# Performance work log

Measured on AMD Instinct MI355X. Metric: run time of the kernel, lower is better.

The kernel has to match this reference:

```python
import jax, jax.numpy as jnp
import numpy as np

N = 100000   # nodes
E = 1600000  # edges
B = 128      # graphs
VOCAB, EMB, HID = 10000, 128, 128


def gcn_conv(x, src, dst, ew, W, b, n_nodes):
    # PyG GCNConv: x' = D^{-1/2}(A_w + I) D^{-1/2} (x W) + b, self-loop weight 1
    x = x @ W  # [N, H]
    loop = jnp.arange(n_nodes)
    src2 = jnp.concatenate([src, loop])
    dst2 = jnp.concatenate([dst, loop])
    ew2 = jnp.concatenate([ew, jnp.ones((n_nodes,), x.dtype)])
    deg = jax.ops.segment_sum(ew2, dst2, num_segments=n_nodes)
    dinv = jnp.where(deg > 0, deg ** -0.5, 0.0)
    norm = dinv[src2] * ew2 * dinv[dst2]                      # [E+N]
    msg = x[src2] * norm[:, None]                             # gather-scale
    out = jax.ops.segment_sum(msg, dst2, num_segments=n_nodes)  # scatter-add
    return out + b


def setup_inputs() -> dict:
    key = jax.random.key(0)
    ks = jax.random.split(key, 12)
    x_idx = jax.random.randint(ks[0], (N,), 0, VOCAB)
    edge_index = jax.random.randint(ks[1], (2, E), 0, N)
    edge_weight = jax.random.uniform(ks[2], (E,), jnp.float32)
    batch = jnp.sort(jax.random.randint(ks[3], (N,), 0, B))
    emb_table = jax.random.normal(ks[4], (VOCAB, EMB), jnp.float32)
    emb_table = emb_table.at[0].set(0.0)  # padding_idx=0
    s = 1.0 / np.sqrt(EMB)
    W1 = jax.random.uniform(ks[5], (EMB, HID), jnp.float32, -s, s)
    b1 = jnp.zeros((HID,), jnp.float32)
    W2 = jax.random.uniform(ks[6], (HID, HID), jnp.float32, -s, s)
    b2 = jnp.zeros((HID,), jnp.float32)
    mlp_W1 = jax.random.uniform(ks[7], (HID, HID // 2), jnp.float32, -s, s)
    mlp_b1 = jax.random.uniform(ks[8], (HID // 2,), jnp.float32, -s, s)
    s2 = 1.0 / np.sqrt(HID // 2)
    mlp_W2 = jax.random.uniform(ks[9], (HID // 2, 2), jnp.float32, -s2, s2)
    mlp_b2 = jax.random.uniform(ks[10], (2,), jnp.float32, -s2, s2)
    return dict(x_idx=x_idx, edge_index=edge_index, edge_weight=edge_weight,
                batch=batch, emb_table=emb_table, W1=W1, b1=b1, W2=W2, b2=b2,
                mlp_W1=mlp_W1, mlp_b1=mlp_b1, mlp_W2=mlp_W2, mlp_b2=mlp_b2)


def reference(x_idx, edge_index, edge_weight, batch, emb_table, W1, b1, W2, b2,
              mlp_W1, mlp_b1, mlp_W2, mlp_b2):
    src, dst = edge_index[0], edge_index[1]
    x = emb_table[x_idx]                                  # embedding lookup
    x = jax.nn.relu(gcn_conv(x, src, dst, edge_weight, W1, b1, N))
    # dropout is inference no-op
    x = jax.nn.relu(gcn_conv(x, src, dst, edge_weight, W2, b2, N))
    # global mean pool over graphs
    sums = jax.ops.segment_sum(x, batch, num_segments=B)
    cnts = jax.ops.segment_sum(jnp.ones((N,), x.dtype), batch, num_segments=B)
    g = sums / jnp.maximum(cnts, 1.0)[:, None]            # [B, HID]
    h = jax.nn.relu(g @ mlp_W1 + mlp_b1)
    out = h @ mlp_W2 + mlp_b2
    return jax.nn.softmax(out, axis=1)
```

## Files before the change

kernel.cpp:

```cpp
#include <hip/hip_runtime.h>
#include <hip/hip_bf16.h>

#define NN 100000
#define NE 1600000
#define NB 128
#define NV 10000
#define HD 128

#define NBUCK 391
#define EBLK 256
#define EPB (NE / EBLK)

using bf16x8 = __attribute__((ext_vector_type(8))) short;
using f32x4  = __attribute__((ext_vector_type(4))) float;
typedef __attribute__((ext_vector_type(8))) unsigned short ushortv8;
typedef __attribute__((ext_vector_type(8))) unsigned char ucharv8;
typedef float f32x2 __attribute__((ext_vector_type(2)));

__device__ __forceinline__ float bf2f(unsigned short b) {
  return __uint_as_float((unsigned)b << 16);
}
__device__ __forceinline__ unsigned short f2bf(float f) {
  __hip_bfloat16 h = __float2bfloat16(f);
  return *reinterpret_cast<unsigned short*>(&h);
}
__device__ __forceinline__ unsigned char f2fp8(float f) {
  return (unsigned char)(__builtin_amdgcn_cvt_pk_fp8_f32(f, 0.f, 0, false) & 0xff);
}
__device__ __forceinline__ void acc16(float* acc, uint4 u, float c) {
  f32x2 v;
  v = __builtin_amdgcn_cvt_pk_f32_fp8((int)u.x, false); acc[0] += c*v[0]; acc[1] += c*v[1];
  v = __builtin_amdgcn_cvt_pk_f32_fp8((int)u.x, true);  acc[2] += c*v[0]; acc[3] += c*v[1];
  v = __builtin_amdgcn_cvt_pk_f32_fp8((int)u.y, false); acc[4] += c*v[0]; acc[5] += c*v[1];
  v = __builtin_amdgcn_cvt_pk_f32_fp8((int)u.y, true);  acc[6] += c*v[0]; acc[7] += c*v[1];
  v = __builtin_amdgcn_cvt_pk_f32_fp8((int)u.z, false); acc[8] += c*v[0]; acc[9] += c*v[1];
  v = __builtin_amdgcn_cvt_pk_f32_fp8((int)u.z, true);  acc[10]+= c*v[0]; acc[11]+= c*v[1];
  v = __builtin_amdgcn_cvt_pk_f32_fp8((int)u.w, false); acc[12]+= c*v[0]; acc[13]+= c*v[1];
  v = __builtin_amdgcn_cvt_pk_f32_fp8((int)u.w, true);  acc[14]+= c*v[0]; acc[15]+= c*v[1];
}


__global__ __launch_bounds__(256) void k_bcount(const int* __restrict__ dst,
                                                int* __restrict__ cntmat) {
  __shared__ int h[NBUCK];
  int t = threadIdx.x, blk = blockIdx.x;
  for (int i = t; i < NBUCK; i += 256) h[i] = 0;
  __syncthreads();
  int base = blk * EPB;
  for (int i = t; i < EPB; i += 256) atomicAdd(&h[dst[base + i] >> 8], 1);
  __syncthreads();
  for (int i = t; i < NBUCK; i += 256) cntmat[blk * NBUCK + i] = h[i];
}

__global__ __launch_bounds__(256) void k_cscan(int* __restrict__ cntmat,
                                               int* __restrict__ totals) {
  __shared__ int sh[256];
  int bu = blockIdx.x, t = threadIdx.x;
  int v = cntmat[t * NBUCK + bu];
  sh[t] = v;
  __syncthreads();
  #pragma unroll
  for (int off = 1; off < 256; off <<= 1) {
    int u = (t >= off) ? sh[t - off] : 0;
    __syncthreads();
    sh[t] += u;
    __syncthreads();
  }
  cntmat[t * NBUCK + bu] = sh[t] - v;
  if (t == 255) totals[bu] = sh[255];
}

__global__ __launch_bounds__(512) void k_tscan(const int* __restrict__ totals,
                                               int* __restrict__ bucketBase) {
  __shared__ int sh[512];
  int t = threadIdx.x;
  int v = (t < NBUCK) ? totals[t] : 0;
  sh[t] = v;
  __syncthreads();
  #pragma unroll
  for (int off = 1; off < 512; off <<= 1) {
    int u = (t >= off) ? sh[t - off] : 0;
    __syncthreads();
    sh[t] += u;
    __syncthreads();
  }
  if (t < NBUCK) bucketBase[t] = sh[t] - v;
  if (t == NBUCK - 1) bucketBase[NBUCK] = sh[t];
}

__global__ __launch_bounds__(256) void k_bscatter(const int* __restrict__ src,
                                                  const int* __restrict__ dst,
                                                  const float* __restrict__ ew,
                                                  const int* __restrict__ cntmat,
                                                  const int* __restrict__ bucketBase,
                                                  unsigned char* __restrict__ dloc,
                                                  uint2* __restrict__ spair) {
  __shared__ int off[NBUCK];
  int t = threadIdx.x, blk = blockIdx.x;
  for (int i = t; i < NBUCK; i += 256)
    off[i] = bucketBase[i] + cntmat[blk * NBUCK + i];
  __syncthreads();
  int base = blk * EPB;
  for (int i = t; i < EPB; i += 256) {
    int e = base + i;
    int d = dst[e];
    int pos = atomicAdd(&off[d >> 8], 1);
    dloc[pos] = (unsigned char)(d & 255);
    spair[pos] = make_uint2((unsigned)src[e], __float_as_uint(ew[e]));
  }
}

__global__ __launch_bounds__(256) void k_bdeg(const unsigned char* __restrict__ dloc,
                                              const uint2* __restrict__ spair,
                                              const int* __restrict__ bucketBase,
                                              int* __restrict__ rowptr,
                                              float* __restrict__ dinv) {
  __shared__ int cnt[256];
  __shared__ float ws[256];
  __shared__ int sh[256];
  int bu = blockIdx.x, t = threadIdx.x;
  cnt[t] = 0; ws[t] = 0.f;
  __syncthreads();
  int ebeg = bucketBase[bu], eend = bucketBase[bu + 1];
  for (int e = ebeg + t; e < eend; e += 256) {
    int dl = dloc[e];
    atomicAdd(&cnt[dl], 1);
    atomicAdd(&ws[dl], __uint_as_float(spair[e].y));
  }
  __syncthreads();
  int v = cnt[t];
  sh[t] = v;
  __syncthreads();
  #pragma unroll
  for (int off = 1; off < 256; off <<= 1) {
    int u = (t >= off) ? sh[t - off] : 0;
    __syncthreads();
    sh[t] += u;
    __syncthreads();
  }
  int gid = bu * 256 + t;
  if (gid < NN) {
    rowptr[gid] = ebeg + sh[t] - v;
    dinv[gid] = rsqrtf(1.0f + ws[t]);
  }
  if (gid == NN) rowptr[NN] = NE;
}

__global__ __launch_bounds__(256) void k_bfill(const unsigned char* __restrict__ dloc,
                                               const uint2* __restrict__ spair,
                                               const int* __restrict__ bucketBase,
                                               const int* __restrict__ rowptr,
                                               const float* __restrict__ dinv,
                                               uint2* __restrict__ csr) {
  __shared__ int cnt[256];
  __shared__ float sdv[256];
  __shared__ int srp[256];
  int bu = blockIdx.x, t = threadIdx.x;
  cnt[t] = 0;
  int gid = (bu << 8) + t;
  if (gid < NN) { sdv[t] = dinv[gid]; srp[t] = rowptr[gid]; }
  __syncthreads();
  int ebeg = bucketBase[bu], eend = bucketBase[bu + 1];
  for (int e = ebeg + t; e < eend; e += 256) {
    int dl = dloc[e];
    uint2 p = spair[e];
    int r = atomicAdd(&cnt[dl], 1);
    float nrm = dinv[(int)p.x] * __uint_as_float(p.y) * sdv[dl];
    csr[srp[dl] + r] = make_uint2(p.x, __float_as_uint(nrm));
  }
}

__global__ void k_wprep2(const float* __restrict__ W1, const float* __restrict__ W2,
                         unsigned short* __restrict__ Wt1, unsigned short* __restrict__ Wt2) {
  int t = blockIdx.x * blockDim.x + threadIdx.x;
  const float* W = (t < 16384) ? W1 : W2;
  unsigned short* Wt = (t < 16384) ? Wt1 : Wt2;
  int i = t & 16383;
  int k = i >> 7, n = i & 127;
  Wt[n * 128 + k] = f2bf(W[k * 128 + n]);
}

template <bool AF32>
__global__ __launch_bounds__(256) void k_gemm_mfma(const void* __restrict__ Av,
                                                   const unsigned short* __restrict__ Wt,
                                                   unsigned char* __restrict__ C, int M) {
  __shared__ unsigned char Cs[128][132];
  const int t = threadIdx.x;
  const int wave = t >> 6, lane = t & 63;
  const int lrow = lane & 15, lk = lane >> 4;
  const int row0 = blockIdx.x * 128;
  const int wrow = row0 + wave * 32;

  f32x4 acc[2][8];
  #pragma unroll
  for (int i = 0; i < 2; ++i)
    #pragma unroll
    for (int j = 0; j < 8; ++j) acc[i][j] = (f32x4){0.f, 0.f, 0.f, 0.f};

  #pragma unroll
  for (int kt = 0; kt < 4; ++kt) {
    bf16x8 a[2];
    #pragma unroll
    for (int rt = 0; rt < 2; ++rt) {
      int r = wrow + rt * 16 + lrow;
      bf16x8 av = (bf16x8){0, 0, 0, 0, 0, 0, 0, 0};
      if (r < M) {
        if (AF32) {
          const float* ap = (const float*)Av + (size_t)r * HD + kt * 32 + lk * 8;
          #pragma unroll
          for (int j = 0; j < 8; ++j) av[j] = (short)f2bf(ap[j]);
        } else {
          av = *(const bf16x8*)((const unsigned short*)Av + (size_t)r * HD + kt * 32 + lk * 8);
        }
      }
      a[rt] = av;
    }
    #pragma unroll
    for (int ct = 0; ct < 8; ++ct) {
      bf16x8 b = *(const bf16x8*)(Wt + (size_t)(ct * 16 + lrow) * HD + kt * 32 + lk * 8);
      acc[0][ct] = __builtin_amdgcn_mfma_f32_16x16x32_bf16(a[0], b, acc[0][ct], 0, 0, 0);
      acc[1][ct] = __builtin_amdgcn_mfma_f32_16x16x32_bf16(a[1], b, acc[1][ct], 0, 0, 0);
    }
  }

  #pragma unroll
  for (int rt = 0; rt < 2; ++rt)
    #pragma unroll
    for (int ct = 0; ct < 8; ++ct)
      #pragma unroll
      for (int reg = 0; reg < 4; ++reg) {
        int lr = wave * 32 + rt * 16 + lk * 4 + reg;
        Cs[lr][ct * 16 + lrow] = f2fp8(acc[rt][ct][reg]);
      }
  __syncthreads();

  #pragma unroll
  for (int i = 0; i < 8; ++i) {
    int idx = t + i * 256;
    int r = idx >> 4;
    int c = (idx & 15) * 8;
    int gr = row0 + r;
    if (gr < M)
      *(ucharv8*)(C + (size_t)gr * HD + c) = *(const ucharv8*)&Cs[r][c];
  }
}

template <bool IND, bool POOL>
__global__ __launch_bounds__(256) void k_agg8(const unsigned char* __restrict__ xw,
                                              const int* __restrict__ xidx,
                                              const int* __restrict__ rowptr,
                                              const uint2* __restrict__ csr,
                                              const float* __restrict__ dinv,
                                              const float* __restrict__ bias,
                                              unsigned short* __restrict__ outp,
                                              const int* __restrict__ batch,
                                              float* __restrict__ sums) {
  int t = threadIdx.x;
  int n = blockIdx.x * 32 + (t >> 3);
  int lane = t & 7;
  int beg = rowptr[n], end = rowptr[n + 1];

  int sn = IND ? xidx[n] : n;
  uint4 uself = *(const uint4*)(xw + (size_t)sn * HD + lane * 16);

  float acc[16];
  #pragma unroll
  for (int j = 0; j < 16; ++j) acc[j] = 0.f;

  int e = beg;
  for (; e + 3 < end; e += 4) {
    uint2 p0 = csr[e],     p1 = csr[e + 1];
    uint2 p2 = csr[e + 2], p3 = csr[e + 3];
    int s0 = (int)p0.x, s1 = (int)p1.x, s2 = (int)p2.x, s3 = (int)p3.x;
    if (IND) { s0 = xidx[s0]; s1 = xidx[s1]; s2 = xidx[s2]; s3 = xidx[s3]; }
    float c0 = __uint_as_float(p0.y), c1 = __uint_as_float(p1.y);
    float c2 = __uint_as_float(p2.y), c3 = __uint_as_float(p3.y);
    uint4 u0 = *(const uint4*)(xw + (size_t)s0 * HD + lane * 16);
    uint4 u1 = *(const uint4*)(xw + (size_t)s1 * HD + lane * 16);
    uint4 u2 = *(const uint4*)(xw + (size_t)s2 * HD + lane * 16);
    uint4 u3 = *(const uint4*)(xw + (size_t)s3 * HD + lane * 16);
    acc16(acc, u0, c0); acc16(acc, u1, c1);
    acc16(acc, u2, c2); acc16(acc, u3, c3);
  }
  for (; e < end; ++e) {
    uint2 p0 = csr[e];
    int s0 = (int)p0.x;
    float c0 = __uint_as_float(p0.y);
    if (IND) s0 = xidx[s0];
    uint4 u0 = *(const uint4*)(xw + (size_t)s0 * HD + lane * 16);
    acc16(acc, u0, c0);
  }

  float d = dinv[n];
  acc16(acc, uself, d * d);

  const float4* bp = reinterpret_cast<const float4*>(bias + lane * 16);
  float4 b0 = bp[0], b1 = bp[1], b2 = bp[2], b3 = bp[3];
  float o[16];
  o[0]  = fmaxf(acc[0]  + b0.x, 0.f); o[1]  = fmaxf(acc[1]  + b0.y, 0.f);
  o[2]  = fmaxf(acc[2]  + b0.z, 0.f); o[3]  = fmaxf(acc[3]  + b0.w, 0.f);
  o[4]  = fmaxf(acc[4]  + b1.x, 0.f); o[5]  = fmaxf(acc[5]  + b1.y, 0.f);
  o[6]  = fmaxf(acc[6]  + b1.z, 0.f); o[7]  = fmaxf(acc[7]  + b1.w, 0.f);
  o[8]  = fmaxf(acc[8]  + b2.x, 0.f); o[9]  = fmaxf(acc[9]  + b2.y, 0.f);
  o[10] = fmaxf(acc[10] + b2.z, 0.f); o[11] = fmaxf(acc[11] + b2.w, 0.f);
  o[12] = fmaxf(acc[12] + b3.x, 0.f); o[13] = fmaxf(acc[13] + b3.y, 0.f);
  o[14] = fmaxf(acc[14] + b3.z, 0.f); o[15] = fmaxf(acc[15] + b3.w, 0.f);

  if constexpr (!POOL) {
    ushortv8 r0, r1;
    #pragma unroll
    for (int j = 0; j < 8; ++j) { r0[j] = f2bf(o[j]); r1[j] = f2bf(o[8 + j]); }
    *(ushortv8*)(outp + (size_t)n * HD + lane * 16) = r0;
    *(ushortv8*)(outp + (size_t)n * HD + lane * 16 + 8) = r1;
  } else {
    __shared__ float pool[32][129];
    __shared__ int ib[32];
    int nl = t >> 3;
    #pragma unroll
    for (int j = 0; j < 16; ++j) pool[nl][lane * 16 + j] = o[j];
    if (t < 32) ib[t] = batch[blockIdx.x * 32 + t];
    __syncthreads();
    if (t < 128) {
      float a = 0.f;
      int c = t;
      #pragma unroll 4
      for (int i = 0; i < 32; ++i) {
        a += pool[i][c];
        if (i == 31 || ib[i + 1] != ib[i]) {
          atomicAdd(&sums[(size_t)ib[i] * HD + c], a);
          a = 0.f;
        }
      }
    }
  }
}

__global__ __launch_bounds__(256) void k_zero_counts(float* __restrict__ sums,
                                                     const int* __restrict__ batch,
                                                     float* __restrict__ cnt) {
  int i = blockIdx.x * blockDim.x + threadIdx.x;
  if (i < NB * HD) sums[i] = 0.f;
  if (blockIdx.x == 0 && threadIdx.x < NB) {
    int b = threadIdx.x;
    auto lb = [&](int v) {
      int lo = 0, hi = NN;
      while (lo < hi) { int m = (lo + hi) >> 1; if (batch[m] < v) lo = m + 1; else hi = m; }
      return lo;
    };
    cnt[b] = (float)(lb(b + 1) - lb(b));
  }
}

__global__ __launch_bounds__(64) void k_head(const float* __restrict__ sums,
                                             const float* __restrict__ cnt,
                                             const float* __restrict__ W1,
                                             const float* __restrict__ b1,
                                             const float* __restrict__ W2,
                                             const float* __restrict__ b2,
                                             float* __restrict__ out) {
  int g = blockIdx.x, t = threadIdx.x;
  __shared__ float gv[128];
  __shared__ float h[64];
  __shared__ float logits[2];
  float c = fmaxf(cnt[g], 1.0f);
  gv[t] = sums[g * HD + t] / c;
  gv[t + 64] = sums[g * HD + 64 + t] / c;
  __syncthreads();
  float acc = b1[t];
  for (int k = 0; k < 128; ++k) acc += gv[k] * W1[k * 64 + t];
  h[t] = fmaxf(acc, 0.f);
  __syncthreads();
  if (t < 2) {
    float a = b2[t];
    for (int j = 0; j < 64; ++j) a += h[j] * W2[j * 2 + t];
    logits[t] = a;
  }
  __syncthreads();
  if (t < 2) {
    float m = fmaxf(logits[0], logits[1]);
    float e0 = __expf(logits[0] - m), e1 = __expf(logits[1] - m);
    out[g * 2 + t] = (t == 0 ? e0 : e1) / (e0 + e1);
  }
}

extern "C" void kernel_launch(void* const* d_in, const int* in_sizes, int n_in,
                              void* d_out, int out_size, void* d_ws, size_t ws_size,
                              hipStream_t stream) {
  const int*   x_idx = (const int*)d_in[0];
  const int*   eidx  = (const int*)d_in[1];
  const float* ew    = (const float*)d_in[2];
  const int*   batch = (const int*)d_in[3];
  const float* emb   = (const float*)d_in[4];
  const float* W1    = (const float*)d_in[5];
  const float* b1    = (const float*)d_in[6];
  const float* W2    = (const float*)d_in[7];
  const float* b2    = (const float*)d_in[8];
  const float* mW1   = (const float*)d_in[9];
  const float* mb1   = (const float*)d_in[10];
  const float* mW2   = (const float*)d_in[11];
  const float* mb2   = (const float*)d_in[12];
  const int* src = eidx;
  const int* dst = eidx + NE;
  float* out = (float*)d_out;

  char* ws = (char*)d_ws;
  size_t off = 0;
  auto alloc = [&](size_t bytes) {
    void* p = ws + off;
    off += (bytes + 255) & ~(size_t)255;
    return p;
  };
  int*   cntmat     = (int*)alloc((size_t)EBLK * NBUCK * 4);
  int*   totals     = (int*)alloc((size_t)NBUCK * 4);
  int*   bucketBase = (int*)alloc((size_t)(NBUCK + 1) * 4);
  int*   rowptr     = (int*)alloc((size_t)(NN + 1) * 4);
  float* dinv       = (float*)alloc((size_t)NN * 4);
  uint2* csr        = (uint2*)alloc((size_t)NE * 8);
  unsigned short* Wt1  = (unsigned short*)alloc((size_t)HD * HD * 2);
  unsigned short* Wt2  = (unsigned short*)alloc((size_t)HD * HD * 2);
  unsigned char* embW  = (unsigned char*)alloc((size_t)NV * HD);
  unsigned char* bufA  = (unsigned char*)alloc((size_t)NN * HD);
  float* sums    = (float*)alloc((size_t)NB * HD * 4);
  float* cnt     = (float*)alloc((size_t)NB * 4);
  char* unionReg = (char*)alloc((size_t)NN * HD * 2);
  uint2* spair = (uint2*)unionReg;
  unsigned char* dloc = (unsigned char*)(unionReg + (size_t)NE * 8);
  unsigned short* bufB = (unsigned short*)unionReg;

  k_bcount<<<EBLK, 256, 0, stream>>>(dst, cntmat);
  k_cscan<<<NBUCK, 256, 0, stream>>>(cntmat, totals);
  k_tscan<<<1, 512, 0, stream>>>(totals, bucketBase);
  k_bscatter<<<EBLK, 256, 0, stream>>>(src, dst, ew, cntmat, bucketBase, dloc, spair);
  k_bdeg<<<NBUCK, 256, 0, stream>>>(dloc, spair, bucketBase, rowptr, dinv);
  k_bfill<<<NBUCK, 256, 0, stream>>>(dloc, spair, bucketBase, rowptr, dinv, csr);

  k_wprep2<<<128, 256, 0, stream>>>(W1, W2, Wt1, Wt2);

  k_gemm_mfma<true><<<(NV + 127) / 128, 256, 0, stream>>>(emb, Wt1, embW, NV);

  k_zero_counts<<<64, 256, 0, stream>>>(sums, batch, cnt);

  k_agg8<true, false><<<NN / 32, 256, 0, stream>>>(
      embW, x_idx, rowptr, csr, dinv, b1, bufB, nullptr, nullptr);

  k_gemm_mfma<false><<<(NN + 127) / 128, 256, 0, stream>>>(bufB, Wt2, bufA, NN);
  k_agg8<false, true><<<NN / 32, 256, 0, stream>>>(
      bufA, nullptr, rowptr, csr, dinv, b2, nullptr, batch, sums);

  k_head<<<NB, 64, 0, stream>>>(sums, cnt, mW1, mb1, mW2, mb2, out);
}
```

Measured before the change: 196.5 us.

## Pack CSR entries into 32-bit src+bf16 norm and refine bucket sort granularity

```diff
diff --git a/kernel.cpp b/kernel.cpp
--- a/kernel.cpp
+++ b/kernel.cpp
@@ -7,8 +7,8 @@
 #define NV 10000
 #define HD 128
 
-#define NBUCK 391
-#define EBLK 256
+#define NBUCK 782
+#define EBLK 2000
 #define EPB (NE / EBLK)
 
 using bf16x8 = __attribute__((ext_vector_type(8))) short;
@@ -26,6 +26,12 @@
 }
 __device__ __forceinline__ unsigned char f2fp8(float f) {
   return (unsigned char)(__builtin_amdgcn_cvt_pk_fp8_f32(f, 0.f, 0, false) & 0xff);
+}
+__device__ __forceinline__ unsigned packSN(unsigned s, float v) {
+  return (s << 15) | ((unsigned)f2bf(v) & 0x7fffu);
+}
+__device__ __forceinline__ float unpackN(unsigned u) {
+  return __uint_as_float((u & 0x7fffu) << 16);
 }
 __device__ __forceinline__ void acc16(float* acc, uint4 u, float c) {
   f32x2 v;
@@ -47,17 +53,24 @@
   for (int i = t; i < NBUCK; i += 256) h[i] = 0;
   __syncthreads();
   int base = blk * EPB;
-  for (int i = t; i < EPB; i += 256) atomicAdd(&h[dst[base + i] >> 8], 1);
-  __syncthreads();
-  for (int i = t; i < NBUCK; i += 256) cntmat[blk * NBUCK + i] = h[i];
+  for (int i = t; i < EPB; i += 256) atomicAdd(&h[dst[base + i] >> 7], 1);
+  __syncthreads();
+  for (int i = t; i < NBUCK; i += 256) cntmat[(size_t)blk * NBUCK + i] = h[i];
 }
 
 __global__ __launch_bounds__(256) void k_cscan(int* __restrict__ cntmat,
                                                int* __restrict__ totals) {
   __shared__ int sh[256];
   int bu = blockIdx.x, t = threadIdx.x;
-  int v = cntmat[t * NBUCK + bu];
-  sh[t] = v;
+  int v[8];
+  int base = t * 8, s = 0;
+  #pragma unroll
+  for (int i = 0; i < 8; ++i) {
+    int blk = base + i;
+    v[i] = (blk < EBLK) ? cntmat[(size_t)blk * NBUCK + bu] : 0;
+    s += v[i];
+  }
+  sh[t] = s;
   __syncthreads();
   #pragma unroll
   for (int off = 1; off < 256; off <<= 1) {
@@ -66,19 +79,24 @@
     sh[t] += u;
     __syncthreads();
   }
-  cntmat[t * NBUCK + bu] = sh[t] - v;
-  if (t == 255) totals[bu] = sh[255];
-}
-
-__global__ __launch_bounds__(512) void k_tscan(const int* __restrict__ totals,
-                                               int* __restrict__ bucketBase) {
-  __shared__ int sh[512];
+  int pre = sh[t] - s;
+  #pragma unroll
+  for (int i = 0; i < 8; ++i) {
+    int blk = base + i;
+    if (blk < EBLK) { cntmat[(size_t)blk * NBUCK + bu] = pre; pre += v[i]; }
+  }
+  if (t == 255) totals[bu] = pre;
+}
+
+__global__ __launch_bounds__(1024) void k_tscan(const int* __restrict__ totals,
+                                                int* __restrict__ bucketBase) {
+  __shared__ int sh[1024];
   int t = threadIdx.x;
   int v = (t < NBUCK) ? totals[t] : 0;
   sh[t] = v;
   __syncthreads();
   #pragma unroll
-  for (int off = 1; off < 512; off <<= 1) {
+  for (int off = 1; off < 1024; off <<= 1) {
     int u = (t >= off) ? sh[t - off] : 0;
     __syncthreads();
     sh[t] += u;
@@ -93,80 +111,84 @@
                                                   const float* __restrict__ ew,
                                                   const int* __restrict__ cntmat,
                                                   const int* __restrict__ bucketBase,
-                                                  unsigned char* __restrict__ dloc,
                                                   uint2* __restrict__ spair) {
   __shared__ int off[NBUCK];
   int t = threadIdx.x, blk = blockIdx.x;
   for (int i = t; i < NBUCK; i += 256)
-    off[i] = bucketBase[i] + cntmat[blk * NBUCK + i];
+    off[i] = bucketBase[i] + cntmat[(size_t)blk * NBUCK + i];
   __syncthreads();
   int base = blk * EPB;
   for (int i = t; i < EPB; i += 256) {
     int e = base + i;
     int d = dst[e];
-    int pos = atomicAdd(&off[d >> 8], 1);
-    dloc[pos] = (unsigned char)(d & 255);
-    spair[pos] = make_uint2((unsigned)src[e], __float_as_uint(ew[e]));
-  }
-}
-
-__global__ __launch_bounds__(256) void k_bdeg(const unsigned char* __restrict__ dloc,
-                                              const uint2* __restrict__ spair,
+    unsigned pew = packSN((unsigned)src[e], ew[e]);
+    int pos = atomicAdd(&off[d >> 7], 1);
+    spair[pos] = make_uint2(pew, (unsigned)(d & 127));
+  }
+}
+
+__global__ __launch_bounds__(256) void k_bdeg(const uint2* __restrict__ spair,
                                               const int* __restrict__ bucketBase,
                                               int* __restrict__ rowptr,
                                               float* __restrict__ dinv) {
-  __shared__ int cnt[256];
-  __shared__ float ws[256];
-  __shared__ int sh[256];
+  __shared__ int cnt[128];
+  __shared__ float ws[128];
+  __shared__ int sh[128];
   int bu = blockIdx.x, t = threadIdx.x;
-  cnt[t] = 0; ws[t] = 0.f;
+  if (t < 128) { cnt[t] = 0; ws[t] = 0.f; }
   __syncthreads();
   int ebeg = bucketBase[bu], eend = bucketBase[bu + 1];
   for (int e = ebeg + t; e < eend; e += 256) {
-    int dl = dloc[e];
-    atomicAdd(&cnt[dl], 1);
-    atomicAdd(&ws[dl], __uint_as_float(spair[e].y));
-  }
-  __syncthreads();
-  int v = cnt[t];
-  sh[t] = v;
-  __syncthreads();
-  #pragma unroll
-  for (int off = 1; off < 256; off <<= 1) {
-    int u = (t >= off) ? sh[t - off] : 0;
-    __syncthreads();
-    sh[t] += u;
-    __syncthreads();
-  }
-  int gid = bu * 256 + t;
-  if (gid < NN) {
-    rowptr[gid] = ebeg + sh[t] - v;
-    dinv[gid] = rsqrtf(1.0f + ws[t]);
-  }
-  if (gid == NN) rowptr[NN] = NE;
-}
-
-__global__ __launch_bounds__(256) void k_bfill(const unsigned char* __restrict__ dloc,
-                                               const uint2* __restrict__ spair,
+    uint2 p = spair[e];
+    atomicAdd(&cnt[p.y], 1);
+    atomicAdd(&ws[p.y], unpackN(p.x));
+  }
+  __syncthreads();
+  int v = 0;
+  if (t < 128) { v = cnt[t]; sh[t] = v; }
+  __syncthreads();
+  #pragma unroll
+  for (int off = 1; off < 128; off <<= 1) {
+    int u = 0;
+    if (t < 128 && t >= off) u = sh[t - off];
+    __syncthreads();
+    if (t < 128) sh[t] += u;
+    __syncthreads();
+  }
+  if (t < 128) {
+    int gid = (bu << 7) + t;
+    if (gid < NN) {
+      rowptr[gid] = ebeg + sh[t] - v;
+      dinv[gid] = rsqrtf(1.0f + ws[t]);
+    }
+    if (gid == NN) rowptr[NN] = NE;
+  }
+}
+
+__global__ __launch_bounds__(256) void k_bfill(const uint2* __restrict__ spair,
                                                const int* __restrict__ bucketBase,
                                                const int* __restrict__ rowptr,
                                                const float* __restrict__ dinv,
-                                               uint2* __restrict__ csr) {
-  __shared__ int cnt[256];
-  __shared__ float sdv[256];
-  __shared__ int srp[256];
+                                               unsigned* __restrict__ csr) {
+  __shared__ int cnt[128];
+  __shared__ float sdv[128];
+  __shared__ int srp[128];
   int bu = blockIdx.x, t = threadIdx.x;
-  cnt[t] = 0;
-  int gid = (bu << 8) + t;
-  if (gid < NN) { sdv[t] = dinv[gid]; srp[t] = rowptr[gid]; }
+  if (t < 128) {
+    cnt[t] = 0;
+    int gid = (bu << 7) + t;
+    if (gid < NN) { sdv[t] = dinv[gid]; srp[t] = rowptr[gid]; }
+  }
   __syncthreads();
   int ebeg = bucketBase[bu], eend = bucketBase[bu + 1];
   for (int e = ebeg + t; e < eend; e += 256) {
-    int dl = dloc[e];
     uint2 p = spair[e];
+    int dl = (int)p.y;
+    unsigned s = p.x >> 15;
+    float ewf = unpackN(p.x);
     int r = atomicAdd(&cnt[dl], 1);
-    float nrm = dinv[(int)p.x] * __uint_as_float(p.y) * sdv[dl];
-    csr[srp[dl] + r] = make_uint2(p.x, __float_as_uint(nrm));
+    float nrm = dinv[s] * ewf * sdv[dl];
+    csr[srp[dl] + r] = packSN(s, nrm);
   }
 }
 
@@ -249,7 +271,7 @@
 __global__ __launch_bounds__(256) void k_agg8(const unsigned char* __restrict__ xw,
                                               const int* __restrict__ xidx,
                                               const int* __restrict__ rowptr,
-                                              const uint2* __restrict__ csr,
+                                              const unsigned* __restrict__ csr,
                                               const float* __restrict__ dinv,
                                               const float* __restrict__ bias,
                                               unsigned short* __restrict__ outp,
@@ -268,13 +290,22 @@
   for (int j = 0; j < 16; ++j) acc[j] = 0.f;
 
   int e = beg;
+  int alignEnd = min(end, (beg + 3) & ~3);
+  for (; e < alignEnd; ++e) {
+    unsigned u = csr[e];
+    int s0 = (int)(u >> 15);
+    if (IND) s0 = xidx[s0];
+    float c0 = unpackN(u);
+    uint4 u0 = *(const uint4*)(xw + (size_t)s0 * HD + lane * 16);
+    acc16(acc, u0, c0);
+  }
   for (; e + 3 < end; e += 4) {
-    uint2 p0 = csr[e],     p1 = csr[e + 1];
-    uint2 p2 = csr[e + 2], p3 = csr[e + 3];
-    int s0 = (int)p0.x, s1 = (int)p1.x, s2 = (int)p2.x, s3 = (int)p3.x;
+    uint4 q = *(const uint4*)(csr + e);
+    int s0 = (int)(q.x >> 15), s1 = (int)(q.y >> 15);
+    int s2 = (int)(q.z >> 15), s3 = (int)(q.w >> 15);
     if (IND) { s0 = xidx[s0]; s1 = xidx[s1]; s2 = xidx[s2]; s3 = xidx[s3]; }
-    float c0 = __uint_as_float(p0.y), c1 = __uint_as_float(p1.y);
-    float c2 = __uint_as_float(p2.y), c3 = __uint_as_float(p3.y);
+    float c0 = unpackN(q.x), c1 = unpackN(q.y);
+    float c2 = unpackN(q.z), c3 = unpackN(q.w);
     uint4 u0 = *(const uint4*)(xw + (size_t)s0 * HD + lane * 16);
     uint4 u1 = *(const uint4*)(xw + (size_t)s1 * HD + lane * 16);
     uint4 u2 = *(const uint4*)(xw + (size_t)s2 * HD + lane * 16);
@@ -283,10 +314,10 @@
     acc16(acc, u2, c2); acc16(acc, u3, c3);
   }
   for (; e < end; ++e) {
-    uint2 p0 = csr[e];
-    int s0 = (int)p0.x;
-    float c0 = __uint_as_float(p0.y);
+    unsigned u = csr[e];
+    int s0 = (int)(u >> 15);
     if (IND) s0 = xidx[s0];
+    float c0 = unpackN(u);
     uint4 u0 = *(const uint4*)(xw + (size_t)s0 * HD + lane * 16);
     acc16(acc, u0, c0);
   }
@@ -415,7 +446,7 @@
   int*   bucketBase = (int*)alloc((size_t)(NBUCK + 1) * 4);
   int*   rowptr     = (int*)alloc((size_t)(NN + 1) * 4);
   float* dinv       = (float*)alloc((size_t)NN * 4);
-  uint2* csr        = (uint2*)alloc((size_t)NE * 8);
+  unsigned* csr     = (unsigned*)alloc((size_t)NE * 4);
   unsigned short* Wt1  = (unsigned short*)alloc((size_t)HD * HD * 2);
   unsigned short* Wt2  = (unsigned short*)alloc((size_t)HD * HD * 2);
   unsigned char* embW  = (unsigned char*)alloc((size_t)NV * HD);
@@ -424,15 +455,14 @@
   float* cnt     = (float*)alloc((size_t)NB * 4);
   char* unionReg = (char*)alloc((size_t)NN * HD * 2);
   uint2* spair = (uint2*)unionReg;
-  unsigned char* dloc = (unsigned char*)(unionReg + (size_t)NE * 8);
   unsigned short* bufB = (unsigned short*)unionReg;
 
   k_bcount<<<EBLK, 256, 0, stream>>>(dst, cntmat);
   k_cscan<<<NBUCK, 256, 0, stream>>>(cntmat, totals);
-  k_tscan<<<1, 512, 0, stream>>>(totals, bucketBase);
-  k_bscatter<<<EBLK, 256, 0, stream>>>(src, dst, ew, cntmat, bucketBase, dloc, spair);
-  k_bdeg<<<NBUCK, 256, 0, stream>>>(dloc, spair, bucketBase, rowptr, dinv);
-  k_bfill<<<NBUCK, 256, 0, stream>>>(dloc, spair, bucketBase, rowptr, dinv, csr);
+  k_tscan<<<1, 1024, 0, stream>>>(totals, bucketBase);
+  k_bscatter<<<EBLK, 256, 0, stream>>>(src, dst, ew, cntmat, bucketBase, spair);
+  k_bdeg<<<NBUCK, 256, 0, stream>>>(spair, bucketBase, rowptr, dinv);
+  k_bfill<<<NBUCK, 256, 0, stream>>>(spair, bucketBase, rowptr, dinv, csr);
 
   k_wprep2<<<128, 256, 0, stream>>>(W1, W2, Wt1, Wt2);
 
```

Measured after the change: 222.2 us. 13.1% more time.
